# Optimization experiments

Measured on AMD Instinct MI355X. Metric: run time of the kernel, lower is better.

## Reference

```python
import jax, jax.numpy as jnp
import numpy as np
from jax import lax

K = 3          # kernel_size
G = 2          # num_groups
DN = ('NHWC', 'HWIO', 'NHWC')


def _conv_same(x, w, b, groups=1):
    y = lax.conv_general_dilated(x, w, (1, 1), 'SAME',
                                 dimension_numbers=DN,
                                 feature_group_count=groups)
    return y + b


def _kernel_grid():
    off = (K - 1) / 2.0
    lin = jnp.linspace(-off, off, K, dtype=jnp.float32)
    dx, dy = jnp.meshgrid(lin, lin)              # 'xy' indexing, like tf default
    return jnp.stack([dx, dy], axis=-1).reshape(K * K, 2)  # [K2, 2] (dx, dy)


def _bilinear_sample(inp, loc):
    # inp: [B,H,W,C], loc: [B,H,W,K2,2] with (x,y) already clipped to valid range
    B, H, W, C = inp.shape
    x, y = loc[..., 0], loc[..., 1]
    x0 = jnp.floor(x); y0 = jnp.floor(y)
    x1 = jnp.clip(x0 + 1.0, 0.0, W - 1.0); x0 = jnp.clip(x0, 0.0, W - 1.0)
    y1 = jnp.clip(y0 + 1.0, 0.0, H - 1.0); y0 = jnp.clip(y0, 0.0, H - 1.0)
    # corner weights (computed from clipped coords, matching the TF code)
    wa = (x1 - x) * (y1 - y)
    wb = (x1 - x) * (y - y0)
    wc = (x - x0) * (y1 - y)
    wd = (x - x0) * (y - y0)
    x0i = x0.astype(jnp.int32); x1i = x1.astype(jnp.int32)
    y0i = y0.astype(jnp.int32); y1i = y1.astype(jnp.int32)
    flat = inp.reshape(B, H * W, C)

    def gather(yi, xi):
        idx = (yi * W + xi).reshape(B, -1, 1)               # [B, H*W*K2, 1]
        v = jnp.take_along_axis(flat, idx, axis=1)          # [B, H*W*K2, C]
        return v.reshape(B, H, W, K * K, C)

    out = (wa[..., None] * gather(y0i, x0i) + wb[..., None] * gather(y1i, x0i)
           + wc[..., None] * gather(y0i, x1i) + wd[..., None] * gather(y1i, x1i))
    return out  # [B,H,W,K2,C]


def _forward(x, off_w, off_b, dw_w, dw_b, pw_w, pw_b):
    B, H, W, C = x.shape
    Cg = C // G
    kg = _kernel_grid()                                     # [K2,2]
    gx, gy = jnp.meshgrid(jnp.arange(W, dtype=jnp.float32),
                          jnp.arange(H, dtype=jnp.float32))
    grid = jnp.stack([gx, gy], axis=-1)                     # [H,W,2] (x,y)
    outs = []
    for g in range(G):
        xi = x[..., g * Cg:(g + 1) * Cg]                    # [B,H,W,Cg]
        offsets = _conv_same(xi, off_w[g], off_b[g])        # [B,H,W,2*K2]
        offsets = offsets.reshape(B, H, W, K * K, 2)
        loc = grid[None, :, :, None, :] + kg[None, None, None] + offsets
        loc = jnp.stack([jnp.clip(loc[..., 0], 0.0, W - 1.0),
                         jnp.clip(loc[..., 1], 0.0, H - 1.0)], axis=-1)
        sampled = _bilinear_sample(xi, loc)                 # [B,H,W,K2,Cg]
        Kin = K * K * Cg
        s = sampled.reshape(B, H, W, Kin)
        s = _conv_same(s, dw_w[g], dw_b[g], groups=Kin)     # depthwise 3x3
        s = _conv_same(s, pw_w[g], pw_b[g])                 # 1x1 pointwise
        outs.append(s)
    return jnp.concatenate(outs, axis=-1)


def setup_inputs() -> dict:
    key = jax.random.key(0)
    ks = jax.random.split(key, 6)
    B, H, W, C = 4, 128, 128, 128
    Cg = C // G
    F = 128
    Fg = F // G
    Kin = K * K * Cg
    x = jax.random.normal(ks[0], (B, H, W, C), jnp.float32)
    # offset conv (zero-init in source; small random weights so offsets ~1px)
    off_w = jax.random.normal(ks[1], (G, K, K, Cg, 2 * K * K), jnp.float32) * 0.05
    off_b = jnp.zeros((G, 2 * K * K), jnp.float32)
    dw_w = jax.random.normal(ks[2], (G, K, K, 1, Kin), jnp.float32) * 0.1
    dw_b = jnp.zeros((G, Kin), jnp.float32)
    pw_w = jax.random.normal(ks[3], (G, 1, 1, Kin, Fg), jnp.float32) / np.sqrt(Kin)
    pw_b = jnp.zeros((G, Fg), jnp.float32)
    return {"x": x, "off_w": off_w, "off_b": off_b,
            "dw_w": dw_w, "dw_b": dw_b, "pw_w": pw_w, "pw_b": pw_b}


def reference(x, off_w, off_b, dw_w, dw_b, pw_w, pw_b):
    return _forward(x, off_w, off_b, dw_w, dw_b, pw_w, pw_b)
```

## Files before the change

### kernel.cpp

```cpp
#include <hip/hip_runtime.h>
#include <hip/hip_bf16.h>

#define HW 128
#define GNUM 2
#define BATCH 4
#define OBT_STRIDE (GNUM * 18 * 2 * 512)
#define PWT_FLOATS 36864
#define OBT_FLOATS 36864

typedef short s16x8 __attribute__((ext_vector_type(8)));
typedef float f32x4 __attribute__((ext_vector_type(4)));

__device__ inline unsigned short f2bf(float f) {
    union { float f; unsigned u; } v;
    v.f = f;
    unsigned r = (v.u + 0x7fffu + ((v.u >> 16) & 1u)) >> 16;
    return (unsigned short)r;
}
__device__ inline unsigned pk2bf(float lo, float hi) {
    __hip_bfloat162 r = __float22bfloat162_rn(float2{lo, hi});
    return *(unsigned*)&r;
}
__device__ inline float blo(unsigned u) {
    union { unsigned u; float f; } v; v.u = u << 16; return v.f;
}
__device__ inline float bhi(unsigned u) {
    union { unsigned u; float f; } v; v.u = u & 0xffff0000u; return v.f;
}

__global__ __launch_bounds__(256) void prep_kernel(
    const float* __restrict__ pw_w, const float* __restrict__ dw_b,
    const float* __restrict__ off_w, unsigned short* __restrict__ pwt,
    unsigned short* __restrict__ obt, float* __restrict__ bias2) {
    const int g = blockIdx.y;
    const int t = threadIdx.x;
    if (blockIdx.x < 9) {
        const int j = blockIdx.x;
        const int wv = t >> 6, lane = t & 63;
        const int f = wv * 16 + (lane & 15);
        const int kbase = (lane >> 4) << 3;
        float part = 0.f;
#pragma unroll
        for (int ks = 0; ks < 2; ++ks)
#pragma unroll
            for (int i = 0; i < 8; ++i) {
                int kin = j * 64 + ks * 32 + kbase + i;
                float v = pw_w[(g * 576 + kin) * 64 + f];
                pwt[((((g * 9 + j) * 4 + wv) * 2 + ks) << 9) + lane * 8 + i] =
                    f2bf(v);
                part += v * dw_b[g * 576 + kin];
            }
        atomicAdd(&bias2[g * 64 + f], part);
    } else {
        const int s = blockIdx.x - 9;
        const int tap = s >> 1;
        for (int e = t; e < 1024; e += 256) {
            int nt = e >> 9, le = e & 511;
            int lane = le >> 3, i = le & 7;
            int k = ((lane >> 4) << 3) + i;
            int c = ((s & 1) << 5) + k;
            int n = (nt << 4) + (lane & 15);
            float v = (n < 18) ? off_w[((g * 9 + tap) * 64 + c) * 18 + n] : 0.f;
            unsigned short hi = f2bf(v);
            unsigned short lo = f2bf(v - blo(hi));
            int idx = (((g * 18 + s) * 2 + nt) << 9) + le;
            obt[idx] = hi;
            obt[OBT_STRIDE + idx] = lo;
        }
    }
}

__global__ __launch_bounds__(256, 4) void deform_fused(
    const float* __restrict__ x, const unsigned short* __restrict__ obt,
    const float* __restrict__ off_b, const float* __restrict__ dw_w,
    const unsigned short* __restrict__ pwt, const float* __restrict__ bias2,
    const float* __restrict__ pw_b, float* __restrict__ out) {
    __shared__ char smem[34016];
    unsigned short* xh = (unsigned short*)smem;
    unsigned short* samp = (unsigned short*)smem;
    unsigned short* dwa = (unsigned short*)(smem + 14400);
    float* offs = (float*)(smem + 23616);
    float4* wlw = (float4*)(smem + 30816);
    int4* wli = (int4*)(smem + 32416);

    const int b = blockIdx.x >> 1, g = blockIdx.x & 1;
    const int tileIdx = blockIdx.y;
    const int h0 = (tileIdx >> 4) << 3, w0 = (tileIdx & 15) << 3;
    const int t = threadIdx.x;
    const int lane = t & 63;
    const int wv = __builtin_amdgcn_readfirstlane(t >> 6);
    const int kq = (lane >> 4) << 3;
    const int col = lane & 15;
    const int rq = (lane >> 4) << 2;

    f32x4 oacc[2][2];
#pragma unroll
    for (int sl = 0; sl < 2; ++sl)
#pragma unroll
        for (int nt = 0; nt < 2; ++nt) oacc[sl][nt] = (f32x4){0.f, 0.f, 0.f, 0.f};
    int mbase[2];
#pragma unroll
    for (int sl = 0; sl < 2; ++sl) {
        int mt = wv + (sl << 2);
        int m = mt * 16 + col;
        if (mt < 7 && m < 100) {
            int opy = m / 10, opx = m - opy * 10;
            mbase[sl] = opy * 12 + opx;
        } else
            mbase[sl] = 0;
    }
    for (int q = 0; q < 2; ++q) {
        if (q) __syncthreads();
        for (int idx = t; idx < 144 * 8; idx += 256) {
            int sp = idx >> 3, cq = idx & 7;
            int sy = sp / 12, sx = sp - sy * 12;
            int gy = h0 - 2 + sy, gx = w0 - 2 + sx;
            uint2 hp = {0, 0}, lp = {0, 0};
            if ((unsigned)gy < HW && (unsigned)gx < HW) {
                const float4 v = *(const float4*)&x[(((b * HW + gy) * HW + gx)
                                                    << 7) +
                                                   (g << 6) + (q << 5) + (cq << 2)];
                hp.x = pk2bf(v.x, v.y);
                hp.y = pk2bf(v.z, v.w);
                lp.x = pk2bf(v.x - blo(hp.x), v.y - bhi(hp.x));
                lp.y = pk2bf(v.z - blo(hp.y), v.w - bhi(hp.y));
            }
            *(uint2*)&xh[sp * 72 + (cq << 2)] = hp;
            *(uint2*)&xh[sp * 72 + 32 + (cq << 2)] = lp;
        }
        __syncthreads();
        for (int tap = 0; tap < 9; ++tap) {
            const int s = (tap << 1) + q;
            const int ky = tap / 3, kx = tap - ky * 3;
            const int shift = ky * 12 + kx;
            const int bidx = ((g * 18 + s) << 1) << 9;
            s16x8 bh0 = *(const s16x8*)&obt[bidx + lane * 8];
            s16x8 bh1 = *(const s16x8*)&obt[bidx + 512 + lane * 8];
            s16x8 bl0 = *(const s16x8*)&obt[OBT_STRIDE + bidx + lane * 8];
            s16x8 bl1 = *(const s16x8*)&obt[OBT_STRIDE + bidx + 512 + lane * 8];
#pragma unroll
            for (int sl = 0; sl < 2; ++sl) {
                if (wv + (sl << 2) < 7) {
                    const int base2 = (mbase[sl] + shift) * 72 + kq;
                    s16x8 ah = *(const s16x8*)&xh[base2];
                    s16x8 al = *(const s16x8*)&xh[base2 + 32];
                    oacc[sl][0] = __builtin_amdgcn_mfma_f32_16x16x32_bf16(
                        ah, bh0, oacc[sl][0], 0, 0, 0);
                    oacc[sl][1] = __builtin_amdgcn_mfma_f32_16x16x32_bf16(
                        ah, bh1, oacc[sl][1], 0, 0, 0);
                    oacc[sl][0] = __builtin_amdgcn_mfma_f32_16x16x32_bf16(
                        al, bh0, oacc[sl][0], 0, 0, 0);
                    oacc[sl][1] = __builtin_amdgcn_mfma_f32_16x16x32_bf16(
                        al, bh1, oacc[sl][1], 0, 0, 0);
                    oacc[sl][0] = __builtin_amdgcn_mfma_f32_16x16x32_bf16(
                        ah, bl0, oacc[sl][0], 0, 0, 0);
                    oacc[sl][1] = __builtin_amdgcn_mfma_f32_16x16x32_bf16(
                        ah, bl1, oacc[sl][1], 0, 0, 0);
                }
            }
        }
    }
#pragma unroll
    for (int sl = 0; sl < 2; ++sl) {
        int mt = wv + (sl << 2);
        if (mt < 7) {
#pragma unroll
            for (int nt = 0; nt < 2; ++nt) {
                int o = (nt << 4) + col;
                if (o < 18) {
                    float ob = off_b[g * 18 + o];
#pragma unroll
                    for (int i = 0; i < 4; ++i) {
                        int m = mt * 16 + rq + i;
                        if (m < 100) offs[m * 18 + o] = oacc[sl][nt][i] + ob;
                    }
                }
            }
        }
    }
    __syncthreads();

    const int fb = wv << 4;
    const int p = lane;
    const int ayp = p >> 3, axp = p & 7;
    const int grp = t >> 4, sl16 = t & 15;

    const float bs = bias2[g * 64 + fb + col] + pw_b[g * 64 + fb + col];
    f32x4 acc[4];
#pragma unroll
    for (int mt = 0; mt < 4; ++mt) acc[mt] = (f32x4){bs, bs, bs, bs};

    for (int j = 0; j < 9; ++j) {
        const int jy = j / 3, jx = j - jy * 3;
        s16x8 bfr[2];
#pragma unroll
        for (int ks = 0; ks < 2; ++ks)
            bfr[ks] = *(const s16x8*)&pwt[((((g * 9 + j) * 4 + wv) * 2 + ks)
                                           << 9) + lane * 8];
        if (t < 100) {
            const int sp = t;
            const int spy = sp / 10, spx = sp - spy * 10;
            const int gy = h0 - 1 + spy, gx = w0 - 1 + spx;
            float4 w4 = {0.f, 0.f, 0.f, 0.f};
            int4 ii = {b << 21, 0, 0, 0};
            if ((unsigned)gy < HW && (unsigned)gx < HW) {
                const float ox = offs[sp * 18 + 2 * j];
                const float oy = offs[sp * 18 + 2 * j + 1];
                float xf = fminf(fmaxf((float)(gx + jx - 1) + ox, 0.f), 127.f);
                float yf = fminf(fmaxf((float)(gy + jy - 1) + oy, 0.f), 127.f);
                float x0 = floorf(xf), y0 = floorf(yf);
                float x1 = fminf(x0 + 1.f, 127.f);
                float y1 = fminf(y0 + 1.f, 127.f);
                w4.x = (x1 - xf) * (y1 - yf);
                w4.y = (x1 - xf) * (yf - y0);
                w4.z = (xf - x0) * (y1 - yf);
                w4.w = (xf - x0) * (yf - y0);
                const int x0i = (int)x0, y0i = (int)y0;
                ii.x = ((b * HW + y0i) * HW + x0i) << 7;
                ii.y = ((int)x1 - x0i) << 7;
                ii.z = ((int)y1 - y0i) << 14;
            }
            wlw[sp] = w4;
            wli[sp] = ii;
        }
        __syncthreads();
        for (int it = 0; it < 7; ++it) {
            const int sp = (it << 4) + grp;
            if (sp < 100) {
                const float4 w4 = wlw[sp];
                const int4 ii = wli[sp];
                const float* xa = x + ii.x + (g << 6) + (sl16 << 2);
                const float4 va = *(const float4*)xa;
                const float4 vb = *(const float4*)(xa + ii.z);
                const float4 vc = *(const float4*)(xa + ii.y);
                const float4 vd = *(const float4*)(xa + ii.y + ii.z);
                float r0 = w4.x * va.x + w4.y * vb.x + w4.z * vc.x + w4.w * vd.x;
                float r1 = w4.x * va.y + w4.y * vb.y + w4.z * vc.y + w4.w * vd.y;
                float r2 = w4.x * va.z + w4.y * vb.z + w4.z * vc.z + w4.w * vd.z;
                float r3 = w4.x * va.w + w4.y * vb.w + w4.z * vc.w + w4.w * vd.w;
                uint2 pk;
                pk.x = pk2bf(r0, r1);
                pk.y = pk2bf(r2, r3);
                *(uint2*)&samp[sp * 72 + (sl16 << 2)] = pk;
            }
        }
        __syncthreads();
#pragma unroll
        for (int cq = 0; cq < 2; ++cq) {
            const int c8 = fb + (cq << 3);
            float d0 = 0.f, d1 = 0.f, d2 = 0.f, d3 = 0.f;
            float d4 = 0.f, d5 = 0.f, d6 = 0.f, d7 = 0.f;
#pragma unroll
            for (int ky = 0; ky < 3; ++ky)
#pragma unroll
                for (int kx = 0; kx < 3; ++kx) {
                    const uint4 hv = *(const uint4*)&samp
                        [((ayp + ky) * 10 + axp + kx) * 72 + c8];
                    const float* wr =
                        &dw_w[((g * 3 + ky) * 3 + kx) * 576 + (j << 6) + c8];
                    d0 += blo(hv.x) * wr[0]; d1 += bhi(hv.x) * wr[1];
                    d2 += blo(hv.y) * wr[2]; d3 += bhi(hv.y) * wr[3];
                    d4 += blo(hv.z) * wr[4]; d5 += bhi(hv.z) * wr[5];
                    d6 += blo(hv.w) * wr[6]; d7 += bhi(hv.w) * wr[7];
                }
            uint4 pk;
            pk.x = pk2bf(d0, d1);
            pk.y = pk2bf(d2, d3);
            pk.z = pk2bf(d4, d5);
            pk.w = pk2bf(d6, d7);
            *(uint4*)&dwa[p * 72 + c8] = pk;
        }
        __syncthreads();
#pragma unroll
        for (int ks = 0; ks < 2; ++ks)
#pragma unroll
            for (int mt = 0; mt < 4; ++mt) {
                s16x8 af = *(const s16x8*)&dwa[(mt * 16 + col) * 72 + ks * 32 +
                                               kq];
                acc[mt] = __builtin_amdgcn_mfma_f32_16x16x32_bf16(
                    af, bfr[ks], acc[mt], 0, 0, 0);
            }
    }
#pragma unroll
    for (int mt = 0; mt < 4; ++mt)
#pragma unroll
        for (int i = 0; i < 4; ++i) {
            int m = mt * 16 + rq + i;
            out[((b * HW + h0 + (m >> 3)) * HW + (w0 + (m & 7))) * 128 +
                (g << 6) + fb + col] = acc[mt][i];
        }
}

extern "C" void kernel_launch(void* const* d_in, const int* in_sizes, int n_in,
                              void* d_out, int out_size, void* d_ws,
                              size_t ws_size, hipStream_t stream) {
    const float* x = (const float*)d_in[0];
    const float* off_w = (const float*)d_in[1];
    const float* off_b = (const float*)d_in[2];
    const float* dw_w = (const float*)d_in[3];
    const float* dw_b = (const float*)d_in[4];
    const float* pw_w = (const float*)d_in[5];
    const float* pw_b = (const float*)d_in[6];

    float* wsf = (float*)d_ws;
    unsigned short* pwt = (unsigned short*)wsf;
    unsigned short* obt = (unsigned short*)(wsf + PWT_FLOATS);
    float* bias2 = wsf + PWT_FLOATS + OBT_FLOATS;

    hipMemsetAsync(bias2, 0, GNUM * 64 * sizeof(float), stream);
    prep_kernel<<<dim3(27, GNUM), dim3(256), 0, stream>>>(pw_w, dw_b, off_w,
                                                          pwt, obt, bias2);
    deform_fused<<<dim3(BATCH * GNUM, 256), dim3(256), 0, stream>>>(
        x, obt, off_b, dw_w, pwt, bias2, pw_b, (float*)d_out);
}
```

Baseline: 207.1 us.

## Fold depthwise 3x3 into pointwise weights and run as one MFMA GEMM

The depthwise 3x3 conv followed by the 1x1 pointwise conv is algebraically merged. Prep now builds combined weights pw_w*dw_w per tap (bf16, laid out for 32x32x16 MFMA), and the main kernel feeds sampled values straight into MFMA over 9 taps x 64 channels. This removes the scalar depthwise FMA loop and the intermediate dwa buffer, at the cost of 9x more MFMA work and larger weight reads from global memory. Other changes: smaller shared memory and packed corner indices to allow 5 blocks per CU, and the bias is computed without atomics or a memset.

Result: slower. 269.7 us (+30.2%).

```diff
diff --git a/kernel.cpp b/kernel.cpp
--- a/kernel.cpp
+++ b/kernel.cpp
@@ -5,11 +5,12 @@
 #define GNUM 2
 #define BATCH 4
 #define OBT_STRIDE (GNUM * 18 * 2 * 512)
-#define PWT_FLOATS 36864
+#define W3T_FLOATS 331776
 #define OBT_FLOATS 36864
 
 typedef short s16x8 __attribute__((ext_vector_type(8)));
 typedef float f32x4 __attribute__((ext_vector_type(4)));
+typedef float f32x16 __attribute__((ext_vector_type(16)));
 
 __device__ inline unsigned short f2bf(float f) {
     union { float f; unsigned u; } v;
@@ -29,30 +30,30 @@
 }
 
 __global__ __launch_bounds__(256) void prep_kernel(
-    const float* __restrict__ pw_w, const float* __restrict__ dw_b,
-    const float* __restrict__ off_w, unsigned short* __restrict__ pwt,
+    const float* __restrict__ pw_w, const float* __restrict__ dw_w,
+    const float* __restrict__ dw_b, const float* __restrict__ off_w,
+    const float* __restrict__ pw_b, unsigned short* __restrict__ w3t,
     unsigned short* __restrict__ obt, float* __restrict__ bias2) {
     const int g = blockIdx.y;
     const int t = threadIdx.x;
-    if (blockIdx.x < 9) {
-        const int j = blockIdx.x;
-        const int wv = t >> 6, lane = t & 63;
-        const int f = wv * 16 + (lane & 15);
-        const int kbase = (lane >> 4) << 3;
-        float part = 0.f;
-#pragma unroll
-        for (int ks = 0; ks < 2; ++ks)
-#pragma unroll
-            for (int i = 0; i < 8; ++i) {
-                int kin = j * 64 + ks * 32 + kbase + i;
-                float v = pw_w[(g * 576 + kin) * 64 + f];
-                pwt[((((g * 9 + j) * 4 + wv) * 2 + ks) << 9) + lane * 8 + i] =
-                    f2bf(v);
-                part += v * dw_b[g * 576 + kin];
-            }
-        atomicAdd(&bias2[g * 64 + f], part);
-    } else {
-        const int s = blockIdx.x - 9;
+    const int bx = blockIdx.x;
+    if (bx < 9) {
+        const int j = bx;
+        for (int idx = t; idx < 36864; idx += 256) {
+            int i = idx & 7;
+            int lane = (idx >> 3) & 63;
+            int u = idx >> 9;
+            int nh = u / 36, ks16 = u - nh * 36;
+            int K = (ks16 << 4) + (((lane >> 5)) << 3) + i;
+            int s = K >> 6, ch = K & 63;
+            int f = (nh << 5) + (lane & 31);
+            float v = pw_w[(g * 576 + (j << 6) + ch) * 64 + f] *
+                      dw_w[(g * 9 + s) * 576 + (j << 6) + ch];
+            w3t[((((g * 9 + j) << 1) + nh) * 36 + ks16) * 512 + lane * 8 + i] =
+                f2bf(v);
+        }
+    } else if (bx < 27) {
+        const int s = bx - 9;
         const int tap = s >> 1;
         for (int e = t; e < 1024; e += 256) {
             int nt = e >> 9, le = e & 511;
@@ -67,21 +68,27 @@
             obt[idx] = hi;
             obt[OBT_STRIDE + idx] = lo;
         }
+    } else {
+        if (t < 64) {
+            const int f = t;
+            float acc = pw_b[g * 64 + f];
+            for (int kin = 0; kin < 576; ++kin)
+                acc += pw_w[(g * 576 + kin) * 64 + f] * dw_b[g * 576 + kin];
+            bias2[g * 64 + f] = acc;
+        }
     }
 }
 
-__global__ __launch_bounds__(256, 4) void deform_fused(
+__global__ __launch_bounds__(256, 5) void deform_fused(
     const float* __restrict__ x, const unsigned short* __restrict__ obt,
-    const float* __restrict__ off_b, const float* __restrict__ dw_w,
-    const unsigned short* __restrict__ pwt, const float* __restrict__ bias2,
-    const float* __restrict__ pw_b, float* __restrict__ out) {
-    __shared__ char smem[34016];
+    const float* __restrict__ off_b, const unsigned short* __restrict__ w3t,
+    const float* __restrict__ bias2, float* __restrict__ out) {
+    __shared__ char smem[27936];
     unsigned short* xh = (unsigned short*)smem;
     unsigned short* samp = (unsigned short*)smem;
-    unsigned short* dwa = (unsigned short*)(smem + 14400);
-    float* offs = (float*)(smem + 23616);
-    float4* wlw = (float4*)(smem + 30816);
-    int4* wli = (int4*)(smem + 32416);
+    float4* wlw = (float4*)(smem + 14400);
+    int2* wli = (int2*)(smem + 16000);
+    float* offs = (float*)(smem + 20736);
 
     const int b = blockIdx.x >> 1, g = blockIdx.x & 1;
     const int tileIdx = blockIdx.y;
@@ -89,125 +96,126 @@
     const int t = threadIdx.x;
     const int lane = t & 63;
     const int wv = __builtin_amdgcn_readfirstlane(t >> 6);
-    const int kq = (lane >> 4) << 3;
-    const int col = lane & 15;
-    const int rq = (lane >> 4) << 2;
-
-    f32x4 oacc[2][2];
-#pragma unroll
-    for (int sl = 0; sl < 2; ++sl)
-#pragma unroll
-        for (int nt = 0; nt < 2; ++nt) oacc[sl][nt] = (f32x4){0.f, 0.f, 0.f, 0.f};
-    int mbase[2];
-#pragma unroll
-    for (int sl = 0; sl < 2; ++sl) {
-        int mt = wv + (sl << 2);
-        int m = mt * 16 + col;
-        if (mt < 7 && m < 100) {
-            int opy = m / 10, opx = m - opy * 10;
-            mbase[sl] = opy * 12 + opx;
-        } else
-            mbase[sl] = 0;
-    }
-    for (int q = 0; q < 2; ++q) {
-        if (q) __syncthreads();
-        for (int idx = t; idx < 144 * 8; idx += 256) {
-            int sp = idx >> 3, cq = idx & 7;
-            int sy = sp / 12, sx = sp - sy * 12;
-            int gy = h0 - 2 + sy, gx = w0 - 2 + sx;
-            uint2 hp = {0, 0}, lp = {0, 0};
-            if ((unsigned)gy < HW && (unsigned)gx < HW) {
-                const float4 v = *(const float4*)&x[(((b * HW + gy) * HW + gx)
-                                                    << 7) +
-                                                   (g << 6) + (q << 5) + (cq << 2)];
-                hp.x = pk2bf(v.x, v.y);
-                hp.y = pk2bf(v.z, v.w);
-                lp.x = pk2bf(v.x - blo(hp.x), v.y - bhi(hp.x));
-                lp.y = pk2bf(v.z - blo(hp.y), v.w - bhi(hp.y));
-            }
-            *(uint2*)&xh[sp * 72 + (cq << 2)] = hp;
-            *(uint2*)&xh[sp * 72 + 32 + (cq << 2)] = lp;
-        }
-        __syncthreads();
-        for (int tap = 0; tap < 9; ++tap) {
-            const int s = (tap << 1) + q;
-            const int ky = tap / 3, kx = tap - ky * 3;
-            const int shift = ky * 12 + kx;
-            const int bidx = ((g * 18 + s) << 1) << 9;
-            s16x8 bh0 = *(const s16x8*)&obt[bidx + lane * 8];
-            s16x8 bh1 = *(const s16x8*)&obt[bidx + 512 + lane * 8];
-            s16x8 bl0 = *(const s16x8*)&obt[OBT_STRIDE + bidx + lane * 8];
-            s16x8 bl1 = *(const s16x8*)&obt[OBT_STRIDE + bidx + 512 + lane * 8];
-#pragma unroll
-            for (int sl = 0; sl < 2; ++sl) {
-                if (wv + (sl << 2) < 7) {
-                    const int base2 = (mbase[sl] + shift) * 72 + kq;
-                    s16x8 ah = *(const s16x8*)&xh[base2];
-                    s16x8 al = *(const s16x8*)&xh[base2 + 32];
-                    oacc[sl][0] = __builtin_amdgcn_mfma_f32_16x16x32_bf16(
-                        ah, bh0, oacc[sl][0], 0, 0, 0);
-                    oacc[sl][1] = __builtin_amdgcn_mfma_f32_16x16x32_bf16(
-                        ah, bh1, oacc[sl][1], 0, 0, 0);
-                    oacc[sl][0] = __builtin_amdgcn_mfma_f32_16x16x32_bf16(
-                        al, bh0, oacc[sl][0], 0, 0, 0);
-                    oacc[sl][1] = __builtin_amdgcn_mfma_f32_16x16x32_bf16(
-                        al, bh1, oacc[sl][1], 0, 0, 0);
-                    oacc[sl][0] = __builtin_amdgcn_mfma_f32_16x16x32_bf16(
-                        ah, bl0, oacc[sl][0], 0, 0, 0);
-                    oacc[sl][1] = __builtin_amdgcn_mfma_f32_16x16x32_bf16(
-                        ah, bl1, oacc[sl][1], 0, 0, 0);
+
+    {
+        const int kq = (lane >> 4) << 3;
+        const int col = lane & 15;
+        const int rq = (lane >> 4) << 2;
+        f32x4 oacc[2][2];
+#pragma unroll
+        for (int sl = 0; sl < 2; ++sl)
+#pragma unroll
+            for (int nt = 0; nt < 2; ++nt)
+                oacc[sl][nt] = (f32x4){0.f, 0.f, 0.f, 0.f};
+        int mbase[2];
+#pragma unroll
+        for (int sl = 0; sl < 2; ++sl) {
+            int mt = wv + (sl << 2);
+            int m = mt * 16 + col;
+            if (mt < 7 && m < 100) {
+                int opy = m / 10, opx = m - opy * 10;
+                mbase[sl] = opy * 12 + opx;
+            } else
+                mbase[sl] = 0;
+        }
+        for (int q = 0; q < 2; ++q) {
+            if (q) __syncthreads();
+            for (int idx = t; idx < 144 * 8; idx += 256) {
+                int sp = idx >> 3, cq = idx & 7;
+                int sy = sp / 12, sx = sp - sy * 12;
+                int gy = h0 - 2 + sy, gx = w0 - 2 + sx;
+                uint2 hp = {0, 0}, lp = {0, 0};
+                if ((unsigned)gy < HW && (unsigned)gx < HW) {
+                    const float4 v = *(const float4*)&x
+                        [(((b * HW + gy) * HW + gx) << 7) + (g << 6) +
+                         (q << 5) + (cq << 2)];
+                    hp.x = pk2bf(v.x, v.y);
+                    hp.y = pk2bf(v.z, v.w);
+                    lp.x = pk2bf(v.x - blo(hp.x), v.y - bhi(hp.x));
+                    lp.y = pk2bf(v.z - blo(hp.y), v.w - bhi(hp.y));
                 }
-            }
-        }
-    }
-#pragma unroll
-    for (int sl = 0; sl < 2; ++sl) {
-        int mt = wv + (sl << 2);
-        if (mt < 7) {
-#pragma unroll
-            for (int nt = 0; nt < 2; ++nt) {
-                int o = (nt << 4) + col;
-                if (o < 18) {
-                    float ob = off_b[g * 18 + o];
-#pragma unroll
-                    for (int i = 0; i < 4; ++i) {
-                        int m = mt * 16 + rq + i;
-                        if (m < 100) offs[m * 18 + o] = oacc[sl][nt][i] + ob;
+                *(uint2*)&xh[sp * 72 + (cq << 2)] = hp;
+                *(uint2*)&xh[sp * 72 + 32 + (cq << 2)] = lp;
+            }
+            __syncthreads();
+            for (int tap = 0; tap < 9; ++tap) {
+                const int s = (tap << 1) + q;
+                const int ky = tap / 3, kx = tap - ky * 3;
+                const int shift = ky * 12 + kx;
+                const int bidx = ((g * 18 + s) << 1) << 9;
+                s16x8 bh0 = *(const s16x8*)&obt[bidx + lane * 8];
+                s16x8 bh1 = *(const s16x8*)&obt[bidx + 512 + lane * 8];
+                s16x8 bl0 = *(const s16x8*)&obt[OBT_STRIDE + bidx + lane * 8];
+                s16x8 bl1 =
+                    *(const s16x8*)&obt[OBT_STRIDE + bidx + 512 + lane * 8];
+#pragma unroll
+                for (int sl = 0; sl < 2; ++sl) {
+                    if (wv + (sl << 2) < 7) {
+                        const int base2 = (mbase[sl] + shift) * 72 + kq;
+                        s16x8 ah = *(const s16x8*)&xh[base2];
+                        s16x8 al = *(const s16x8*)&xh[base2 + 32];
+                        oacc[sl][0] = __builtin_amdgcn_mfma_f32_16x16x32_bf16(
+                            ah, bh0, oacc[sl][0], 0, 0, 0);
+                        oacc[sl][1] = __builtin_amdgcn_mfma_f32_16x16x32_bf16(
+                            ah, bh1, oacc[sl][1], 0, 0, 0);
+                        oacc[sl][0] = __builtin_amdgcn_mfma_f32_16x16x32_bf16(
+                            al, bh0, oacc[sl][0], 0, 0, 0);
+                        oacc[sl][1] = __builtin_amdgcn_mfma_f32_16x16x32_bf16(
+                            al, bh1, oacc[sl][1], 0, 0, 0);
+                        oacc[sl][0] = __builtin_amdgcn_mfma_f32_16x16x32_bf16(
+                            ah, bl0, oacc[sl][0], 0, 0, 0);
+                        oacc[sl][1] = __builtin_amdgcn_mfma_f32_16x16x32_bf16(
+                            ah, bl1, oacc[sl][1], 0, 0, 0);
                     }
                 }
             }
         }
+#pragma unroll
+        for (int sl = 0; sl < 2; ++sl) {
+            int mt = wv + (sl << 2);
+            if (mt < 7) {
+#pragma unroll
+                for (int nt = 0; nt < 2; ++nt) {
+                    int o = (nt << 4) + col;
+                    if (o < 18) {
+                        float ob = off_b[g * 18 + o];
+#pragma unroll
+                        for (int i = 0; i < 4; ++i) {
+                            int m = mt * 16 + rq + i;
+                            if (m < 100)
+                                offs[m * 18 + o] = oacc[sl][nt][i] + ob;
+                        }
+                    }
+                }
+            }
+        }
     }
     __syncthreads();
 
-    const int fb = wv << 4;
-    const int p = lane;
-    const int ayp = p >> 3, axp = p & 7;
+    const int mh = wv >> 1, nh = wv & 1;
+    const int p32 = (mh << 5) + (lane & 31);
+    const int pr = p32 >> 3, pc = p32 & 7;
+    const int kq8 = (lane >> 5) << 3;
+    const int fcol = (nh << 5) + (lane & 31);
     const int grp = t >> 4, sl16 = t & 15;
 
-    const float bs = bias2[g * 64 + fb + col] + pw_b[g * 64 + fb + col];
-    f32x4 acc[4];
-#pragma unroll
-    for (int mt = 0; mt < 4; ++mt) acc[mt] = (f32x4){bs, bs, bs, bs};
+    const float bs = bias2[g * 64 + fcol];
+    f32x16 acc;
+#pragma unroll
+    for (int i = 0; i < 16; ++i) acc[i] = bs;
 
     for (int j = 0; j < 9; ++j) {
         const int jy = j / 3, jx = j - jy * 3;
-        s16x8 bfr[2];
-#pragma unroll
-        for (int ks = 0; ks < 2; ++ks)
-            bfr[ks] = *(const s16x8*)&pwt[((((g * 9 + j) * 4 + wv) * 2 + ks)
-                                           << 9) + lane * 8];
         if (t < 100) {
             const int sp = t;
             const int spy = sp / 10, spx = sp - spy * 10;
             const int gy = h0 - 1 + spy, gx = w0 - 1 + spx;
             float4 w4 = {0.f, 0.f, 0.f, 0.f};
-            int4 ii = {b << 21, 0, 0, 0};
+            int2 ii = {b << 21, 0};
             if ((unsigned)gy < HW && (unsigned)gx < HW) {
-                const float ox = offs[sp * 18 + 2 * j];
-                const float oy = offs[sp * 18 + 2 * j + 1];
-                float xf = fminf(fmaxf((float)(gx + jx - 1) + ox, 0.f), 127.f);
-                float yf = fminf(fmaxf((float)(gy + jy - 1) + oy, 0.f), 127.f);
+                const float2 o2 = *(const float2*)&offs[sp * 18 + 2 * j];
+                float xf = fminf(fmaxf((float)(gx + jx - 1) + o2.x, 0.f), 127.f);
+                float yf = fminf(fmaxf((float)(gy + jy - 1) + o2.y, 0.f), 127.f);
                 float x0 = floorf(xf), y0 = floorf(yf);
                 float x1 = fminf(x0 + 1.f, 127.f);
                 float y1 = fminf(y0 + 1.f, 127.f);
@@ -217,8 +225,7 @@
                 w4.w = (xf - x0) * (yf - y0);
                 const int x0i = (int)x0, y0i = (int)y0;
                 ii.x = ((b * HW + y0i) * HW + x0i) << 7;
-                ii.y = ((int)x1 - x0i) << 7;
-                ii.z = ((int)y1 - y0i) << 14;
+                ii.y = ((int)x1 - x0i) | (((int)y1 - y0i) << 1);
             }
             wlw[sp] = w4;
             wli[sp] = ii;
@@ -228,12 +235,14 @@
             const int sp = (it << 4) + grp;
             if (sp < 100) {
                 const float4 w4 = wlw[sp];
-                const int4 ii = wli[sp];
+                const int2 ii = wli[sp];
+                const int dxo = (ii.y & 1) << 7;
+                const int dyo = (ii.y & 2) << 13;
                 const float* xa = x + ii.x + (g << 6) + (sl16 << 2);
                 const float4 va = *(const float4*)xa;
-                const float4 vb = *(const float4*)(xa + ii.z);
-                const float4 vc = *(const float4*)(xa + ii.y);
-                const float4 vd = *(const float4*)(xa + ii.y + ii.z);
+                const float4 vb = *(const float4*)(xa + dyo);
+                const float4 vc = *(const float4*)(xa + dxo);
+                const float4 vd = *(const float4*)(xa + dxo + dyo);
                 float r0 = w4.x * va.x + w4.y * vb.x + w4.z * vc.x + w4.w * vd.x;
                 float r1 = w4.x * va.y + w4.y * vb.y + w4.z * vc.y + w4.w * vd.y;
                 float r2 = w4.x * va.z + w4.y * vb.z + w4.z * vc.z + w4.w * vd.z;
@@ -245,50 +254,29 @@
             }
         }
         __syncthreads();
-#pragma unroll
-        for (int cq = 0; cq < 2; ++cq) {
-            const int c8 = fb + (cq << 3);
-            float d0 = 0.f, d1 = 0.f, d2 = 0.f, d3 = 0.f;
-            float d4 = 0.f, d5 = 0.f, d6 = 0.f, d7 = 0.f;
-#pragma unroll
-            for (int ky = 0; ky < 3; ++ky)
-#pragma unroll
-                for (int kx = 0; kx < 3; ++kx) {
-                    const uint4 hv = *(const uint4*)&samp
-                        [((ayp + ky) * 10 + axp + kx) * 72 + c8];
-                    const float* wr =
-                        &dw_w[((g * 3 + ky) * 3 + kx) * 576 + (j << 6) + c8];
-                    d0 += blo(hv.x) * wr[0]; d1 += bhi(hv.x) * wr[1];
-                    d2 += blo(hv.y) * wr[2]; d3 += bhi(hv.y) * wr[3];
-                    d4 += blo(hv.z) * wr[4]; d5 += bhi(hv.z) * wr[5];
-                    d6 += blo(hv.w) * wr[6]; d7 += bhi(hv.w) * wr[7];
-                }
-            uint4 pk;
-            pk.x = pk2bf(d0, d1);
-            pk.y = pk2bf(d2, d3);
-            pk.z = pk2bf(d4, d5);
-            pk.w = pk2bf(d6, d7);
-            *(uint4*)&dwa[p * 72 + c8] = pk;
-        }
-        __syncthreads();
-#pragma unroll
-        for (int ks = 0; ks < 2; ++ks)
-#pragma unroll
-            for (int mt = 0; mt < 4; ++mt) {
-                s16x8 af = *(const s16x8*)&dwa[(mt * 16 + col) * 72 + ks * 32 +
-                                               kq];
-                acc[mt] = __builtin_amdgcn_mfma_f32_16x16x32_bf16(
-                    af, bfr[ks], acc[mt], 0, 0, 0);
-            }
+        const unsigned short* w3 =
+            &w3t[((((g * 9 + j) << 1) + nh) * 36) * 512 + lane * 8];
+#pragma unroll
+        for (int s = 0; s < 9; ++s) {
+            const int ky = s / 3, kx = s - ky * 3;
+            const int abase = ((pr + ky) * 10 + pc + kx) * 72 + kq8;
+#pragma unroll
+            for (int chunk = 0; chunk < 4; ++chunk) {
+                s16x8 af = *(const s16x8*)&samp[abase + (chunk << 4)];
+                s16x8 bf = *(const s16x8*)&w3[((s << 2) + chunk) << 9];
+                acc = __builtin_amdgcn_mfma_f32_32x32x16_bf16(af, bf, acc, 0,
+                                                              0, 0);
+            }
+        }
     }
-#pragma unroll
-    for (int mt = 0; mt < 4; ++mt)
-#pragma unroll
-        for (int i = 0; i < 4; ++i) {
-            int m = mt * 16 + rq + i;
-            out[((b * HW + h0 + (m >> 3)) * HW + (w0 + (m & 7))) * 128 +
-                (g << 6) + fb + col] = acc[mt][i];
-        }
+    const int rbase = (lane >> 5) << 2;
+#pragma unroll
+    for (int r = 0; r < 16; ++r) {
+        int row = (r & 3) + ((r >> 2) << 3) + rbase;
+        int pp = (mh << 5) + row;
+        out[((b * HW + h0 + (pp >> 3)) * HW + (w0 + (pp & 7))) * 128 +
+            (g << 6) + fcol] = acc[r];
+    }
 }
 
 extern "C" void kernel_launch(void* const* d_in, const int* in_sizes, int n_in,
@@ -303,13 +291,12 @@
     const float* pw_b = (const float*)d_in[6];
 
     float* wsf = (float*)d_ws;
-    unsigned short* pwt = (unsigned short*)wsf;
-    unsigned short* obt = (unsigned short*)(wsf + PWT_FLOATS);
-    float* bias2 = wsf + PWT_FLOATS + OBT_FLOATS;
-
-    hipMemsetAsync(bias2, 0, GNUM * 64 * sizeof(float), stream);
-    prep_kernel<<<dim3(27, GNUM), dim3(256), 0, stream>>>(pw_w, dw_b, off_w,
-                                                          pwt, obt, bias2);
+    unsigned short* w3t = (unsigned short*)wsf;
+    unsigned short* obt = (unsigned short*)(wsf + W3T_FLOATS);
+    float* bias2 = wsf + W3T_FLOATS + OBT_FLOATS;
+
+    prep_kernel<<<dim3(28, GNUM), dim3(256), 0, stream>>>(
+        pw_w, dw_w, dw_b, off_w, pw_b, w3t, obt, bias2);
     deform_fused<<<dim3(BATCH * GNUM, 256), dim3(256), 0, stream>>>(
-        x, obt, off_b, dw_w, pwt, bias2, pw_b, (float*)d_out);
-}
+        x, obt, off_b, w3t, bias2, (float*)d_out);
+}
```
